# Performance work log

Measured on AMD Instinct MI355X. Metric: run time of the kernel, lower is better.

Reference implementation:

```python
import jax, jax.numpy as jnp
import numpy as np

E = 1024      # embedding_size
K = 64        # key_size
D = 64        # head_size
S = 1024      # context_size
V = 32000     # vocab_size
H = 16        # layer_size (heads per layer)
L = 8         # num_layers
B = 2


def _pe():
    pos = jnp.arange(S, dtype=jnp.float32)[:, None]
    i = jnp.arange(E, dtype=jnp.float32)[None, :]
    ang = pos / jnp.power(10000.0, 2.0 * i / E)
    return jnp.where((jnp.arange(E) % 2 == 0)[None, :], jnp.sin(ang), jnp.cos(ang))


def setup_inputs() -> dict:
    key = jax.random.key(0)
    ks = iter(jax.random.split(key, 32))
    s = 0.02
    n = lambda shape: jax.random.normal(next(ks), shape, dtype=jnp.float32) * s
    inp = {
        "tokens": jax.random.randint(next(ks), (B, S), 0, V),
        "emb": n((V, E)),
        "pe": _pe(),
        "k1w": n((L, H, K, E)), "k1b": n((L, H, K)),
        "k2w": n((L, H, K, K)), "k2b": n((L, H, K)),
        "q1w": n((L, H, K, E)), "q1b": n((L, H, K)),
        "q2w": n((L, H, K, K)), "q2b": n((L, H, K)),
        "vw": n((L, H, D, E)), "vb": n((L, H, D)),
        "lnw": jnp.ones((L, E), jnp.float32), "lnb": jnp.zeros((L, E), jnp.float32),
        "p1w": n((L, E, E)), "p1b": n((L, E)),
        "p2w": n((L, E, E)), "p2b": n((L, E)),
        "predw": n((V, E)), "predb": n((V,)),
    }
    return inp


def reference(tokens, emb, pe, k1w, k1b, k2w, k2b, q1w, q1b, q2w, q2b,
              vw, vb, lnw, lnb, p1w, p1b, p2w, p2b, predw, predb):
    relu = jax.nn.relu
    x = emb[tokens] + pe[:tokens.shape[1]]                       # [B,S,E]
    seq = tokens.shape[1]
    # Faithful to original: tril (past+diag) gets the -1e10 penalty.
    mask = jnp.tril(jnp.ones((seq, seq), x.dtype)) * -1e10
    for l in range(L):
        # two-layer ReLU MLPs for K and Q, batched over heads
        k = relu(jnp.einsum('bse,hke->bhsk', x, k1w[l]) + k1b[l][None, :, None, :])
        k = relu(jnp.einsum('bhsk,hjk->bhsj', k, k2w[l]) + k2b[l][None, :, None, :])
        q = relu(jnp.einsum('bse,hke->bhsk', x, q1w[l]) + q1b[l][None, :, None, :])
        q = relu(jnp.einsum('bhsk,hjk->bhsj', q, q2w[l]) + q2b[l][None, :, None, :])
        v = jnp.einsum('bse,hde->bhsd', x, vw[l]) + vb[l][None, :, None, :]
        scores = jnp.einsum('bhsk,bhtk->bhst', q, k) / (K ** 0.5) + mask
        w = jax.nn.softmax(scores, axis=-1)
        o = jnp.einsum('bhst,bhtd->bhsd', w, v)                  # [B,H,S,D]
        o = o.transpose(0, 2, 1, 3).reshape(x.shape[0], seq, H * D)
        y = x + o
        mu = y.mean(-1, keepdims=True)
        var = ((y - mu) ** 2).mean(-1, keepdims=True)
        yn = (y - mu) / jnp.sqrt(var + 1e-5) * lnw[l] + lnb[l]
        h1 = relu(yn @ p1w[l].T + p1b[l])
        x = relu(h1 @ p2w[l].T + p2b[l])
    logits = x @ predw.T + predb                                 # [B,S,V]
    return logits
```

## Files before the change

### kernel.cpp

```cpp
#include <hip/hip_runtime.h>


typedef __attribute__((ext_vector_type(8))) short bf16x8;
typedef __attribute__((ext_vector_type(4))) float f32x4;

#define L_ 8
#define S_ 1024
#define E_ 1024
#define B_ 2
#define H_ 16
#define V_ 32000
#define M_ 2048

__device__ __forceinline__ unsigned short f2b(float f) {
  union { float f; unsigned int u; } v; v.f = f;
  unsigned int r = v.u + 0x7FFFu + ((v.u >> 16) & 1u);
  return (unsigned short)(r >> 16);
}

#define GLDS16(gptr, lptr)                                                            \
  __builtin_amdgcn_global_load_lds(                                                   \
      (const __attribute__((address_space(1))) unsigned int*)(gptr),                  \
      (__attribute__((address_space(3))) unsigned int*)(lptr), 16, 0, 0)

__global__ void cvt_kernel(const float* __restrict__ src, unsigned short* __restrict__ dst) {
  size_t i = ((size_t)blockIdx.x * 256 + threadIdx.x) * 4;
  float4 v = *(const float4*)(src + i);
  unsigned short* d = dst + i;
  d[0] = f2b(v.x); d[1] = f2b(v.y); d[2] = f2b(v.z); d[3] = f2b(v.w);
}

__global__ void cvt_seg_kernel(const float* __restrict__ src, unsigned short* __restrict__ dst,
                               int perLayer, int dstStride, int dstOff) {
  size_t i = ((size_t)blockIdx.x * 256 + threadIdx.x) * 4;
  int l = (int)(i / perLayer);
  int off = (int)(i - (size_t)l * perLayer);
  float4 v = *(const float4*)(src + i);
  unsigned short* d = dst + (size_t)l * dstStride + dstOff + off;
  d[0] = f2b(v.x); d[1] = f2b(v.y); d[2] = f2b(v.z); d[3] = f2b(v.w);
}

__global__ void biascat_kernel(const float* __restrict__ k1b, const float* __restrict__ q1b,
                               const float* __restrict__ vb, float* __restrict__ bcat) {
  int i = blockIdx.x * 256 + threadIdx.x;
  int l = i / 3072, j = i - l * 3072;
  float v;
  if (j < 1024)      v = k1b[l * 1024 + j];
  else if (j < 2048) v = q1b[l * 1024 + j - 1024];
  else               v = vb [l * 1024 + j - 2048];
  bcat[i] = v;
}

__global__ void embed_kernel(const int* __restrict__ tokens, const float* __restrict__ emb,
                             const float* __restrict__ pe, float* __restrict__ x32,
                             unsigned short* __restrict__ xb) {
  int row = blockIdx.x;
  int s = row & (S_ - 1);
  int e0 = threadIdx.x * 4;
  int tok = tokens[row];
  float4 ev = *(const float4*)(emb + (size_t)tok * E_ + e0);
  float4 pv = *(const float4*)(pe + (size_t)s * E_ + e0);
  float4 v; v.x = ev.x + pv.x; v.y = ev.y + pv.y; v.z = ev.z + pv.z; v.w = ev.w + pv.w;
  *(float4*)(x32 + (size_t)row * E_ + e0) = v;
  ushort4 o; o.x = f2b(v.x); o.y = f2b(v.y); o.z = f2b(v.z); o.w = f2b(v.w);
  *(ushort4*)(xb + (size_t)row * E_ + e0) = o;
}

template <int BM, int BN, int RELU, int OBF, int OF32, int VT>
__global__ __launch_bounds__(256) void gemm97(
    const unsigned short* __restrict__ A, const unsigned short* __restrict__ W,
    const float* __restrict__ bias, unsigned short* __restrict__ Cb,
    float* __restrict__ Cf, unsigned short* __restrict__ vTp,
    int K, int N, int reluN) {
  constexpr int AR = BM / 64;
  constexpr int BR = BN / 64;
  constexpr int FM = BM / 32;
  constexpr int FN = BN / 32;
  __shared__ __align__(16) unsigned short sA[BM * 32];
  __shared__ __align__(16) unsigned short sB[BN * 32];
  const int tid = threadIdx.x;
  const int lane = tid & 63, wave = tid >> 6;
  const int l16 = lane & 15, lhi = lane >> 4;

  const int gx = gridDim.x, nwg = gx * gridDim.y;
  int o = blockIdx.y * gx + blockIdx.x;
  int wg = ((nwg & 7) == 0) ? ((o & 7) * (nwg >> 3) + (o >> 3)) : o;
  const int row0 = (wg % gx) * BM, col0 = (wg / gx) * BN;

  const int wm = (wave >> 1) * (BM / 2), wn = (wave & 1) * (BN / 2);

  const int srow = wave * 16 + (lane >> 2);
  const int scol = ((lane & 3) ^ ((lane >> 3) & 3)) * 8;
  const int cx = (lhi ^ ((l16 >> 1) & 3)) * 8;

  f32x4 acc[FM][FN] = {};

  for (int k0 = 0; k0 < K; k0 += 32) {
#pragma unroll
    for (int r = 0; r < AR; r++)
      GLDS16(A + (size_t)(row0 + r * 64 + srow) * K + k0 + scol,
             sA + r * 2048 + wave * 512);
#pragma unroll
    for (int r = 0; r < BR; r++)
      GLDS16(W + (size_t)(col0 + r * 64 + srow) * K + k0 + scol,
             sB + r * 2048 + wave * 512);
    __syncthreads();

    bf16x8 af[FM], bf[FN];
#pragma unroll
    for (int i = 0; i < FM; i++)
      af[i] = *(const bf16x8*)(sA + (wm + i * 16 + l16) * 32 + cx);
#pragma unroll
    for (int j = 0; j < FN; j++)
      bf[j] = *(const bf16x8*)(sB + (wn + j * 16 + l16) * 32 + cx);
#pragma unroll
    for (int i = 0; i < FM; i++)
#pragma unroll
      for (int j = 0; j < FN; j++)
        acc[i][j] = __builtin_amdgcn_mfma_f32_16x16x32_bf16(bf[j], af[i], acc[i][j], 0, 0, 0);
    __syncthreads();
  }

#pragma unroll
  for (int j = 0; j < FN; j++) {
    const int colb = col0 + wn + j * 16 + lhi * 4;
    const float4 bv = *(const float4*)(bias + colb);
    const bool dorelu = (RELU == 1) || (RELU == 2 && colb < reluN);
#pragma unroll
    for (int i = 0; i < FM; i++) {
      const int row = row0 + wm + i * 16 + l16;
      float v0 = acc[i][j][0] + bv.x, v1 = acc[i][j][1] + bv.y;
      float v2 = acc[i][j][2] + bv.z, v3 = acc[i][j][3] + bv.w;
      if (dorelu) {
        v0 = fmaxf(v0, 0.f); v1 = fmaxf(v1, 0.f);
        v2 = fmaxf(v2, 0.f); v3 = fmaxf(v3, 0.f);
      }
      if (OBF) {
        ushort4 ob; ob.x = f2b(v0); ob.y = f2b(v1); ob.z = f2b(v2); ob.w = f2b(v3);
        *(ushort4*)(Cb + (size_t)row * N + colb) = ob;
      }
      if (OF32) {
        float4 of; of.x = v0; of.y = v1; of.z = v2; of.w = v3;
        *(float4*)(Cf + (size_t)row * N + colb) = of;
      }
      if (VT) {
        if (colb - lhi * 4 >= 2048) {
          const int hd0 = colb - 2048;
          const int bq = row >> 10, s = row & 1023;
          unsigned short* vr = vTp + ((size_t)(bq << 10) + hd0) * 1024 + s;
          vr[0] = f2b(v0); vr[1024] = f2b(v1); vr[2048] = f2b(v2); vr[3072] = f2b(v3);
        }
      }
    }
  }
}

__global__ __launch_bounds__(512, 2) void gemm256(
    const unsigned short* __restrict__ A, const unsigned short* __restrict__ W,
    const float* __restrict__ bias, float* __restrict__ Cf) {
  constexpr int KK = 1024;
  constexpr int NT = 32;
  __shared__ __align__(16) unsigned short sA[2][8192];
  __shared__ __align__(16) unsigned short sB[2][8192];
  const int tid = threadIdx.x;
  const int lane = tid & 63, wave = tid >> 6;
  const int l16 = lane & 15, lhi = lane >> 4;
  const int wr = wave >> 2, wc = wave & 3;

  const int o = blockIdx.x;
  const int wg = (o & 7) * 125 + (o >> 3);
  const int row0 = (wg & 7) * 256;
  const int col0 = (wg >> 3) * 256;

  const int sr = tid >> 2;
  const int sc = ((tid & 3) ^ ((tid >> 3) & 3)) * 8;
  const int cx = (lhi ^ ((l16 >> 1) & 3)) * 8;

  f32x4 acc[8][4] = {};

  auto stage = [&](int t) {
    const int buf = t & 1;
    const int k0 = t * 32;
#pragma unroll
    for (int is = 0; is < 2; is++) {
      GLDS16(A + (size_t)(row0 + is * 128 + sr) * KK + k0 + sc,
             &sA[buf][(is * 512 + (tid & ~63)) * 8]);
      GLDS16(W + (size_t)(col0 + is * 128 + sr) * KK + k0 + sc,
             &sB[buf][(is * 512 + (tid & ~63)) * 8]);
    }
  };

  stage(0);
  stage(1);

  bf16x8 af[4], bf[4];
  for (int t = 0; t < NT - 1; t++) {
    const int buf = t & 1;
    asm volatile("s_waitcnt vmcnt(4)" ::: "memory");
    __builtin_amdgcn_s_barrier();
    __builtin_amdgcn_sched_barrier(0);
#pragma unroll
    for (int j = 0; j < 4; j++)
      bf[j] = *(const bf16x8*)(&sB[buf][(wc * 64 + j * 16 + l16) * 32 + cx]);
#pragma unroll
    for (int i = 0; i < 4; i++)
      af[i] = *(const bf16x8*)(&sA[buf][(wr * 128 + i * 16 + l16) * 32 + cx]);
    __builtin_amdgcn_s_setprio(1);
#pragma unroll
    for (int i = 0; i < 4; i++)
#pragma unroll
      for (int j = 0; j < 4; j++)
        acc[i][j] = __builtin_amdgcn_mfma_f32_16x16x32_bf16(bf[j], af[i], acc[i][j], 0, 0, 0);
    __builtin_amdgcn_s_setprio(0);
#pragma unroll
    for (int i = 0; i < 4; i++)
      af[i] = *(const bf16x8*)(&sA[buf][(wr * 128 + 64 + i * 16 + l16) * 32 + cx]);
    __builtin_amdgcn_s_setprio(1);
#pragma unroll
    for (int i = 0; i < 4; i++)
#pragma unroll
      for (int j = 0; j < 4; j++)
        acc[i + 4][j] = __builtin_amdgcn_mfma_f32_16x16x32_bf16(bf[j], af[i], acc[i + 4][j], 0, 0, 0);
    __builtin_amdgcn_s_setprio(0);
    __builtin_amdgcn_s_barrier();
    __builtin_amdgcn_sched_barrier(0);
    if (t <= NT - 3) stage(t + 2);
  }
  {
    const int buf = (NT - 1) & 1;
    asm volatile("s_waitcnt vmcnt(0)" ::: "memory");
    __builtin_amdgcn_s_barrier();
    __builtin_amdgcn_sched_barrier(0);
#pragma unroll
    for (int j = 0; j < 4; j++)
      bf[j] = *(const bf16x8*)(&sB[buf][(wc * 64 + j * 16 + l16) * 32 + cx]);
#pragma unroll
    for (int i = 0; i < 4; i++)
      af[i] = *(const bf16x8*)(&sA[buf][(wr * 128 + i * 16 + l16) * 32 + cx]);
    __builtin_amdgcn_s_setprio(1);
#pragma unroll
    for (int i = 0; i < 4; i++)
#pragma unroll
      for (int j = 0; j < 4; j++)
        acc[i][j] = __builtin_amdgcn_mfma_f32_16x16x32_bf16(bf[j], af[i], acc[i][j], 0, 0, 0);
    __builtin_amdgcn_s_setprio(0);
#pragma unroll
    for (int i = 0; i < 4; i++)
      af[i] = *(const bf16x8*)(&sA[buf][(wr * 128 + 64 + i * 16 + l16) * 32 + cx]);
    __builtin_amdgcn_s_setprio(1);
#pragma unroll
    for (int i = 0; i < 4; i++)
#pragma unroll
      for (int j = 0; j < 4; j++)
        acc[i + 4][j] = __builtin_amdgcn_mfma_f32_16x16x32_bf16(bf[j], af[i], acc[i + 4][j], 0, 0, 0);
    __builtin_amdgcn_s_setprio(0);
  }

#pragma unroll
  for (int j = 0; j < 4; j++) {
    const int colb = col0 + wc * 64 + j * 16 + lhi * 4;
    const float4 bv = *(const float4*)(bias + colb);
#pragma unroll
    for (int i = 0; i < 8; i++) {
      const int row = row0 + wr * 128 + i * 16 + l16;
      float4 of;
      of.x = acc[i][j][0] + bv.x; of.y = acc[i][j][1] + bv.y;
      of.z = acc[i][j][2] + bv.z; of.w = acc[i][j][3] + bv.w;
      *(float4*)(Cf + (size_t)row * V_ + colb) = of;
    }
  }
}

__global__ __launch_bounds__(256) void k2q2_kernel(
    const unsigned short* __restrict__ kqv, const unsigned short* __restrict__ wk2,
    const unsigned short* __restrict__ wq2, const float* __restrict__ k2b,
    const float* __restrict__ q2b, unsigned short* __restrict__ kbuf,
    unsigned short* __restrict__ qbuf) {
  const int m0 = blockIdx.x * 64;
  const int h = blockIdx.y;
  const int which = blockIdx.z;
  const unsigned short* Ap = kqv + (which ? 1024 : 0) + h * 64;
  const unsigned short* Wp = (which ? wq2 : wk2) + h * 4096;
  const float* bias = (which ? q2b : k2b) + h * 64;
  unsigned short* out = (which ? qbuf : kbuf) + h * 64;
  const int lane = threadIdx.x & 63, wave = threadIdx.x >> 6;
  const int l16 = lane & 15, lhi = lane >> 4;
  const int mw = m0 + wave * 16;

  f32x4 acc[4] = {};
#pragma unroll
  for (int ks = 0; ks < 2; ks++) {
    bf16x8 a = *(const bf16x8*)(Ap + (size_t)(mw + l16) * 3072 + ks * 32 + (lhi << 3));
#pragma unroll
    for (int j = 0; j < 4; j++) {
      bf16x8 b = *(const bf16x8*)(Wp + (j * 16 + l16) * 64 + ks * 32 + (lhi << 3));
      acc[j] = __builtin_amdgcn_mfma_f32_16x16x32_bf16(a, b, acc[j], 0, 0, 0);
    }
  }
#pragma unroll
  for (int j = 0; j < 4; j++) {
    float bv = bias[j * 16 + l16];
#pragma unroll
    for (int r = 0; r < 4; r++) {
      int row = mw + (lhi << 2) + r;
      float v = fmaxf(acc[j][r] + bv, 0.f);
      out[(size_t)row * 1024 + j * 16 + l16] = f2b(v);
    }
  }
}

__global__ __launch_bounds__(128) void attn_kernel(
    const unsigned short* __restrict__ qbuf,
    const unsigned short* __restrict__ kbuf,
    const unsigned short* __restrict__ vT,
    float* __restrict__ o32) {
  constexpr int LD = 72;
  __shared__ __align__(16) unsigned short sP[2 * 16 * LD];
  const int bid = blockIdx.x;
  const int bh = bid & 31, qt = bid >> 5;
  const int b = bh >> 4, h = bh & 15;
  const int tid = threadIdx.x, lane = tid & 63, w = tid >> 6;
  const int l16 = lane & 15, lhi = lane >> 4;
  const int base = b * S_;
  const int qrow = qt * 32 + w * 16 + l16;

  bf16x8 aq[2];
#pragma unroll
  for (int ks = 0; ks < 2; ks++)
    aq[ks] = *(const bf16x8*)(qbuf + (size_t)(base + qrow) * 1024 + h * 64 + ks * 32 + (lhi << 3));

  f32x4 oacc[4] = {};
  float mrun[4], lrun[4];
#pragma unroll
  for (int r = 0; r < 4; r++) { mrun[r] = -1e10f; lrun[r] = 0.f; }
  const int srow = qt * 32 + w * 16 + (lhi << 2);
  const int t0s = (qt == 31) ? 0 : ((qt >> 1) << 6);

  unsigned short* sPw = sP + w * 16 * LD;

  for (int t0 = t0s; t0 < S_; t0 += 64) {
    f32x4 sacc[4] = {};
#pragma unroll
    for (int ks = 0; ks < 2; ks++) {
#pragma unroll
      for (int nt = 0; nt < 4; nt++) {
        bf16x8 bk = *(const bf16x8*)(kbuf + (size_t)(base + t0 + nt * 16 + l16) * 1024 +
                                     h * 64 + ks * 32 + (lhi << 3));
        sacc[nt] = __builtin_amdgcn_mfma_f32_16x16x32_bf16(aq[ks], bk, sacc[nt], 0, 0, 0);
      }
    }
    float p[4][4];
#pragma unroll
    for (int nt = 0; nt < 4; nt++) {
      int tcol = t0 + nt * 16 + l16;
#pragma unroll
      for (int r = 0; r < 4; r++) {
        float v = sacc[nt][r] * 0.125f;
        if (tcol <= srow + r) v = -1e10f;
        p[nt][r] = v;
      }
    }
#pragma unroll
    for (int r = 0; r < 4; r++) {
      float m = fmaxf(fmaxf(p[0][r], p[1][r]), fmaxf(p[2][r], p[3][r]));
#pragma unroll
      for (int off = 1; off < 16; off <<= 1) m = fmaxf(m, __shfl_xor(m, off, 16));
      float mnew = fmaxf(mrun[r], m);
      float alpha = __expf(mrun[r] - mnew);
      mrun[r] = mnew;
      float rs = 0.f;
#pragma unroll
      for (int nt = 0; nt < 4; nt++) {
        float e = __expf(p[nt][r] - mnew);
        p[nt][r] = e; rs += e;
      }
#pragma unroll
      for (int off = 1; off < 16; off <<= 1) rs += __shfl_xor(rs, off, 16);
      lrun[r] = lrun[r] * alpha + rs;
      oacc[0][r] *= alpha; oacc[1][r] *= alpha; oacc[2][r] *= alpha; oacc[3][r] *= alpha;
    }
#pragma unroll
    for (int nt = 0; nt < 4; nt++)
#pragma unroll
      for (int r = 0; r < 4; r++)
        sPw[((lhi << 2) + r) * LD + nt * 16 + l16] = f2b(p[nt][r]);
#pragma unroll
    for (int ks = 0; ks < 2; ks++) {
      bf16x8 ap = *(const bf16x8*)(sPw + l16 * LD + ks * 32 + (lhi << 3));
#pragma unroll
      for (int nt = 0; nt < 4; nt++) {
        bf16x8 bv = *(const bf16x8*)(vT + (size_t)(bh * 64 + nt * 16 + l16) * 1024 +
                                     t0 + ks * 32 + (lhi << 3));
        oacc[nt] = __builtin_amdgcn_mfma_f32_16x16x32_bf16(ap, bv, oacc[nt], 0, 0, 0);
      }
    }
  }
#pragma unroll
  for (int nt = 0; nt < 4; nt++) {
#pragma unroll
    for (int r = 0; r < 4; r++) {
      int row = srow + r;
      o32[(size_t)(base + row) * 1024 + h * 64 + nt * 16 + l16] = oacc[nt][r] / lrun[r];
    }
  }
}

__global__ __launch_bounds__(256) void ln_kernel(
    const float* __restrict__ x32, const float* __restrict__ o32,
    const float* __restrict__ lnw, const float* __restrict__ lnb,
    unsigned short* __restrict__ yn) {
  __shared__ float red[8];
  const int row = blockIdx.x, tid = threadIdx.x;
  const int lane = tid & 63, wave = tid >> 6;
  const int e0 = tid * 4;
  float4 xv = *(const float4*)(x32 + (size_t)row * E_ + e0);
  float4 ov = *(const float4*)(o32 + (size_t)row * E_ + e0);
  float y0 = xv.x + ov.x, y1 = xv.y + ov.y, y2 = xv.z + ov.z, y3 = xv.w + ov.w;
  float s = y0 + y1 + y2 + y3;
  float sq = y0 * y0 + y1 * y1 + y2 * y2 + y3 * y3;
#pragma unroll
  for (int off = 32; off > 0; off >>= 1) {
    s += __shfl_xor(s, off, 64);
    sq += __shfl_xor(sq, off, 64);
  }
  if (lane == 0) { red[wave * 2] = s; red[wave * 2 + 1] = sq; }
  __syncthreads();
  float ts = red[0] + red[2] + red[4] + red[6];
  float tsq = red[1] + red[3] + red[5] + red[7];
  float mu = ts * (1.f / E_);
  float var = tsq * (1.f / E_) - mu * mu;
  float rstd = rsqrtf(var + 1e-5f);
  float4 gv = *(const float4*)(lnw + e0);
  float4 bv = *(const float4*)(lnb + e0);
  ushort4 o;
  o.x = f2b((y0 - mu) * rstd * gv.x + bv.x);
  o.y = f2b((y1 - mu) * rstd * gv.y + bv.y);
  o.z = f2b((y2 - mu) * rstd * gv.z + bv.z);
  o.w = f2b((y3 - mu) * rstd * gv.w + bv.w);
  *(ushort4*)(yn + (size_t)row * E_ + e0) = o;
}

extern "C" void kernel_launch(void* const* d_in, const int* in_sizes, int n_in,
                              void* d_out, int out_size, void* d_ws, size_t ws_size,
                              hipStream_t stream) {
  const int* tokens  = (const int*)d_in[0];
  const float* emb   = (const float*)d_in[1];
  const float* pe    = (const float*)d_in[2];
  const float* k1w   = (const float*)d_in[3];
  const float* k1b   = (const float*)d_in[4];
  const float* k2w   = (const float*)d_in[5];
  const float* k2b   = (const float*)d_in[6];
  const float* q1w   = (const float*)d_in[7];
  const float* q1b   = (const float*)d_in[8];
  const float* q2w   = (const float*)d_in[9];
  const float* q2b   = (const float*)d_in[10];
  const float* vw    = (const float*)d_in[11];
  const float* vb    = (const float*)d_in[12];
  const float* lnw   = (const float*)d_in[13];
  const float* lnb   = (const float*)d_in[14];
  const float* p1w   = (const float*)d_in[15];
  const float* p1b   = (const float*)d_in[16];
  const float* p2w   = (const float*)d_in[17];
  const float* p2b   = (const float*)d_in[18];
  const float* predw = (const float*)d_in[19];
  const float* predb = (const float*)d_in[20];
  float* out = (float*)d_out;

  char* p = (char*)d_ws;
  auto alloc = [&](size_t bytes) -> char* {
    char* r = p; p += (bytes + 255) & ~(size_t)255; return r;
  };
  unsigned short* wcat  = (unsigned short*)alloc((size_t)L_ * 3072 * 1024 * 2);
  unsigned short* wk2   = (unsigned short*)alloc((size_t)L_ * H_ * 64 * 64 * 2);
  unsigned short* wq2   = (unsigned short*)alloc((size_t)L_ * H_ * 64 * 64 * 2);
  unsigned short* wp1   = (unsigned short*)alloc((size_t)L_ * 1024 * 1024 * 2);
  unsigned short* wp2   = (unsigned short*)alloc((size_t)L_ * 1024 * 1024 * 2);
  unsigned short* wpred = (unsigned short*)alloc((size_t)V_ * 1024 * 2);
  float*          bcat  = (float*)alloc((size_t)L_ * 3072 * 4);
  float*          x32   = (float*)alloc((size_t)M_ * 1024 * 4);
  unsigned short* xb    = (unsigned short*)alloc((size_t)M_ * 1024 * 2);
  unsigned short* kqv   = (unsigned short*)alloc((size_t)M_ * 3072 * 2);
  unsigned short* kbuf  = (unsigned short*)alloc((size_t)M_ * 1024 * 2);
  unsigned short* qbuf  = (unsigned short*)alloc((size_t)M_ * 1024 * 2);
  unsigned short* vTb   = (unsigned short*)alloc((size_t)32 * 64 * 1024 * 2);
  float*          o32   = (float*)alloc((size_t)M_ * 1024 * 4);
  unsigned short* yn    = (unsigned short*)alloc((size_t)M_ * 1024 * 2);
  unsigned short* h1    = (unsigned short*)alloc((size_t)M_ * 1024 * 2);
  if ((size_t)(p - (char*)d_ws) > ws_size) return;

  cvt_seg_kernel<<<8192, 256, 0, stream>>>(k1w, wcat, 1048576, 3145728, 0);
  cvt_seg_kernel<<<8192, 256, 0, stream>>>(q1w, wcat, 1048576, 3145728, 1048576);
  cvt_seg_kernel<<<8192, 256, 0, stream>>>(vw,  wcat, 1048576, 3145728, 2097152);
  cvt_kernel<<<512, 256, 0, stream>>>(k2w, wk2);
  cvt_kernel<<<512, 256, 0, stream>>>(q2w, wq2);
  cvt_kernel<<<8192, 256, 0, stream>>>(p1w, wp1);
  cvt_kernel<<<8192, 256, 0, stream>>>(p2w, wp2);
  cvt_kernel<<<32000, 256, 0, stream>>>(predw, wpred);
  biascat_kernel<<<96, 256, 0, stream>>>(k1b, q1b, vb, bcat);

  embed_kernel<<<M_, 256, 0, stream>>>(tokens, emb, pe, x32, xb);

  for (int l = 0; l < L_; l++) {
    const unsigned short* wcat_l = wcat + (size_t)l * 3072 * 1024;
    const float* bcat_l = bcat + (size_t)l * 3072;
    const unsigned short* wk2_l = wk2 + (size_t)l * H_ * 64 * 64;
    const unsigned short* wq2_l = wq2 + (size_t)l * H_ * 64 * 64;
    const unsigned short* wp1_l = wp1 + (size_t)l * 1024 * 1024;
    const unsigned short* wp2_l = wp2 + (size_t)l * 1024 * 1024;

    gemm97<128, 128, 2, 1, 0, 1><<<dim3(16, 24), 256, 0, stream>>>(
        xb, wcat_l, bcat_l, kqv, nullptr, vTb, 1024, 3072, 2048);
    k2q2_kernel<<<dim3(32, 16, 2), 256, 0, stream>>>(
        kqv, wk2_l, wq2_l, k2b + l * 1024, q2b + l * 1024, kbuf, qbuf);
    attn_kernel<<<1024, 128, 0, stream>>>(qbuf, kbuf, vTb, o32);
    ln_kernel<<<M_, 256, 0, stream>>>(x32, o32, lnw + l * 1024, lnb + l * 1024, yn);
    gemm97<64, 128, 1, 1, 0, 0><<<dim3(32, 8), 256, 0, stream>>>(
        yn, wp1_l, p1b + l * 1024, h1, nullptr, nullptr, 1024, 1024, 0);
    gemm97<64, 128, 1, 1, 1, 0><<<dim3(32, 8), 256, 0, stream>>>(
        h1, wp2_l, p2b + l * 1024, xb, x32, nullptr, 1024, 1024, 0);
  }

  gemm256<<<1000, 512, 0, stream>>>(xb, wpred, predb, out);
}
```

Before: 1.544 ms.

## Triple-buffer LDS in vocab GEMM and drop the trailing barrier per k-step

The 256x256 prediction GEMM goes from double to triple LDS buffering. The prefetch of tile kt+2 is issued inside the compute loop, right after the first A-fragment reads, and the second barrier per iteration is removed. The goal is to overlap global-to-LDS copies with MFMA work and cut barrier stalls. The cost is LDS use growing from 64KB to 96KB per block, which may lower the two-blocks-per-CU occupancy implied by the launch bounds.

```diff
diff --git a/kernel.cpp b/kernel.cpp
--- a/kernel.cpp
+++ b/kernel.cpp
@@ -160,8 +160,8 @@
     const float* __restrict__ bias, float* __restrict__ Cf) {
   constexpr int KK = 1024;
   constexpr int NT = 32;
-  __shared__ __align__(16) unsigned short sA[2][8192];
-  __shared__ __align__(16) unsigned short sB[2][8192];
+  __shared__ __align__(16) unsigned short sA[3][8192];
+  __shared__ __align__(16) unsigned short sB[3][8192];
   const int tid = threadIdx.x;
   const int lane = tid & 63, wave = tid >> 6;
   const int l16 = lane & 15, lhi = lane >> 4;
@@ -172,88 +172,55 @@
   const int row0 = (wg & 7) * 256;
   const int col0 = (wg >> 3) * 256;
 
-  const int sr = tid >> 2;
-  const int sc = ((tid & 3) ^ ((tid >> 3) & 3)) * 8;
-  const int cx = (lhi ^ ((l16 >> 1) & 3)) * 8;
+  const int pr0 = tid >> 2;
+  const int xc = ((tid & 3) ^ ((pr0 >> 1) & 3)) * 8;
+  const int ldsx = (lhi ^ ((l16 >> 1) & 3)) * 8;
 
   f32x4 acc[8][4] = {};
 
-  auto stage = [&](int t) {
-    const int buf = t & 1;
-    const int k0 = t * 32;
+  auto stage = [&](int kt) {
+    const int slot = kt % 3;
+    const int k0 = kt * 32;
 #pragma unroll
     for (int is = 0; is < 2; is++) {
-      GLDS16(A + (size_t)(row0 + is * 128 + sr) * KK + k0 + sc,
-             &sA[buf][(is * 512 + (tid & ~63)) * 8]);
-      GLDS16(W + (size_t)(col0 + is * 128 + sr) * KK + k0 + sc,
-             &sB[buf][(is * 512 + (tid & ~63)) * 8]);
+      GLDS16(A + (size_t)(row0 + is * 128 + pr0) * KK + k0 + xc,
+             &sA[slot][(is * 512 + (tid & ~63)) * 8]);
+      GLDS16(W + (size_t)(col0 + is * 128 + pr0) * KK + k0 + xc,
+             &sB[slot][(is * 512 + (tid & ~63)) * 8]);
     }
   };
 
   stage(0);
   stage(1);
 
-  bf16x8 af[4], bf[4];
-  for (int t = 0; t < NT - 1; t++) {
-    const int buf = t & 1;
-    asm volatile("s_waitcnt vmcnt(4)" ::: "memory");
+  for (int kt = 0; kt < NT; kt++) {
+    const int slot = kt % 3;
+    if (kt == NT - 1) { asm volatile("s_waitcnt vmcnt(0)" ::: "memory"); }
+    else              { asm volatile("s_waitcnt vmcnt(4)" ::: "memory"); }
     __builtin_amdgcn_s_barrier();
     __builtin_amdgcn_sched_barrier(0);
+
+    const unsigned short* sa = &sA[slot][(wr * 128) * 32];
+    const unsigned short* sb = &sB[slot][(wc * 64) * 32];
+    bf16x8 bf[4];
 #pragma unroll
     for (int j = 0; j < 4; j++)
-      bf[j] = *(const bf16x8*)(&sB[buf][(wc * 64 + j * 16 + l16) * 32 + cx]);
-#pragma unroll
-    for (int i = 0; i < 4; i++)
-      af[i] = *(const bf16x8*)(&sA[buf][(wr * 128 + i * 16 + l16) * 32 + cx]);
-    __builtin_amdgcn_s_setprio(1);
-#pragma unroll
-    for (int i = 0; i < 4; i++)
+      bf[j] = *(const bf16x8*)(sb + (j * 16 + l16) * 32 + ldsx);
+
+#pragma unroll
+    for (int ip = 0; ip < 4; ip++) {
+      bf16x8 af0 = *(const bf16x8*)(sa + ((ip * 2) * 16 + l16) * 32 + ldsx);
+      bf16x8 af1 = *(const bf16x8*)(sa + ((ip * 2 + 1) * 16 + l16) * 32 + ldsx);
+      if (ip == 0 && kt + 2 < NT) stage(kt + 2);
+      __builtin_amdgcn_s_setprio(1);
 #pragma unroll
       for (int j = 0; j < 4; j++)
-        acc[i][j] = __builtin_amdgcn_mfma_f32_16x16x32_bf16(bf[j], af[i], acc[i][j], 0, 0, 0);
-    __builtin_amdgcn_s_setprio(0);
-#pragma unroll
-    for (int i = 0; i < 4; i++)
-      af[i] = *(const bf16x8*)(&sA[buf][(wr * 128 + 64 + i * 16 + l16) * 32 + cx]);
-    __builtin_amdgcn_s_setprio(1);
-#pragma unroll
-    for (int i = 0; i < 4; i++)
+        acc[ip * 2][j] = __builtin_amdgcn_mfma_f32_16x16x32_bf16(bf[j], af0, acc[ip * 2][j], 0, 0, 0);
 #pragma unroll
       for (int j = 0; j < 4; j++)
-        acc[i + 4][j] = __builtin_amdgcn_mfma_f32_16x16x32_bf16(bf[j], af[i], acc[i + 4][j], 0, 0, 0);
-    __builtin_amdgcn_s_setprio(0);
-    __builtin_amdgcn_s_barrier();
-    __builtin_amdgcn_sched_barrier(0);
-    if (t <= NT - 3) stage(t + 2);
-  }
-  {
-    const int buf = (NT - 1) & 1;
-    asm volatile("s_waitcnt vmcnt(0)" ::: "memory");
-    __builtin_amdgcn_s_barrier();
-    __builtin_amdgcn_sched_barrier(0);
-#pragma unroll
-    for (int j = 0; j < 4; j++)
-      bf[j] = *(const bf16x8*)(&sB[buf][(wc * 64 + j * 16 + l16) * 32 + cx]);
-#pragma unroll
-    for (int i = 0; i < 4; i++)
-      af[i] = *(const bf16x8*)(&sA[buf][(wr * 128 + i * 16 + l16) * 32 + cx]);
-    __builtin_amdgcn_s_setprio(1);
-#pragma unroll
-    for (int i = 0; i < 4; i++)
-#pragma unroll
-      for (int j = 0; j < 4; j++)
-        acc[i][j] = __builtin_amdgcn_mfma_f32_16x16x32_bf16(bf[j], af[i], acc[i][j], 0, 0, 0);
-    __builtin_amdgcn_s_setprio(0);
-#pragma unroll
-    for (int i = 0; i < 4; i++)
-      af[i] = *(const bf16x8*)(&sA[buf][(wr * 128 + 64 + i * 16 + l16) * 32 + cx]);
-    __builtin_amdgcn_s_setprio(1);
-#pragma unroll
-    for (int i = 0; i < 4; i++)
-#pragma unroll
-      for (int j = 0; j < 4; j++)
-        acc[i + 4][j] = __builtin_amdgcn_mfma_f32_16x16x32_bf16(bf[j], af[i], acc[i + 4][j], 0, 0, 0);
-    __builtin_amdgcn_s_setprio(0);
+        acc[ip * 2 + 1][j] = __builtin_amdgcn_mfma_f32_16x16x32_bf16(bf[j], af1, acc[ip * 2 + 1][j], 0, 0, 0);
+      __builtin_amdgcn_s_setprio(0);
+    }
   }
 
 #pragma unroll
```

After: 1.545 ms. No clear change (+0.1%).
